# Performance work log

Hardware: AMD Instinct MI355X
Metric: run time of the kernel (lower is better)

## Reference

```python
import jax, jax.numpy as jnp
import numpy as np

ALPHA = 0.0
# tetra edge vertex pairs, same order as the original: (0,1),(0,2),(0,3),(1,2),(1,3),(2,3)
EDGE_PAIRS = np.array([[0, 1], [0, 2], [0, 3], [1, 2], [1, 3], [2, 3]], dtype=np.int32)


def setup_inputs() -> dict:
    key = jax.random.key(0)
    B, N, T = 2, 120000, 600000
    k1, k2 = jax.random.split(key)
    pred = jax.random.normal(k1, (B, N, 4), dtype=jnp.float32)
    tetra = jax.random.randint(k2, (B, T, 4), 0, N, dtype=jnp.int32)
    return {"pred": pred, "tetra": tetra}


def _laplace_tetra(verts, faces):
    # verts: [N,4], faces: [T,4] int. For vertex slot j, contribution is
    # sum_{k != j} (v_k - v_j) = (v0+v1+v2+v3) - 4*v_j ; weight 3 per incidence.
    N = verts.shape[0]
    v = verts[faces]                                  # [T,4,4]
    vsum = jnp.sum(v, axis=1, keepdims=True)          # [T,1,4]
    contrib = (vsum - 4.0 * v).reshape(-1, 4)         # [T*4,4]
    idx = faces.reshape(-1)
    term = jax.ops.segment_sum(contrib, idx, num_segments=N)
    norm = jax.ops.segment_sum(jnp.full(idx.shape, 3.0, verts.dtype), idx, num_segments=N)
    term = term / jnp.clip(norm, 1.0)[:, None]
    return jnp.mean(term ** 2)


def reference(pred, tetra):
    tetra = tetra.astype(jnp.int32)
    # center pred over the point dimension (axis=1)
    pred = pred - jnp.mean(pred, axis=1, keepdims=True)

    def per_batch(pre, tetr):
        L1 = _laplace_tetra(pre, tetr)
        Tetrah = pre[tetr]                             # [T,4,4]
        pa = Tetrah[:, EDGE_PAIRS[:, 0], :]            # [T,6,4] edge endpoint 0
        pb = Tetrah[:, EDGE_PAIRS[:, 1], :]            # [T,6,4] edge endpoint 1
        wa = pa[..., 3]
        wb = pb[..., 3]
        edge = (wa - ALPHA) * (wb - ALPHA)             # [T,6]
        L2 = jnp.mean(wa * wb)
        L3 = jnp.mean((jnp.linalg.norm(pa - pb, axis=-1) - 0.4) ** 2)
        # zero-crossing interpolation: x = (alpha - w0)*m/q + x0
        d = pa - pb                                    # [T,6,4]
        q = d[..., 3]
        safe_q = jnp.where(jnp.abs(q) > 1e-12, q, 1.0)
        t = (ALPHA - wa) / safe_q                      # [T,6]
        pts = pa[..., :3] + t[..., None] * d[..., :3]  # [T,6,3]
        mask = edge < 0                                # valid crossing edges
        pts = jnp.where(mask[..., None], pts, 0.0)
        return L1, L2, L3, pts, mask

    L1, L2, L3, pts, mask = jax.vmap(per_batch)(pred, tetra)
    # losses = [L1, L2, L3, L4] (L4 is always 0 in the original)
    losses = jnp.stack([jnp.mean(L1), jnp.mean(L2), jnp.mean(L3), jnp.zeros((), pred.dtype)])
    return losses, pts, mask
```

## Files before the change

### kernel.cpp

```cpp
#include <hip/hip_runtime.h>


#define VPB 2048
#define VPB_SHIFT 11
#define KMAX 120
#define CAP 49152u
#define NPART 8192
#define FP_BIAS 16.0f
#define FP_SCALE 8.0f
#define FP_INV   0.125f
#define FMASK 0x3FFFULL

typedef float vf4  __attribute__((ext_vector_type(4)));
typedef float vf4u __attribute__((ext_vector_type(4), aligned(4)));
typedef int   vi4  __attribute__((ext_vector_type(4)));

__device__ inline double waveReduce(double v) {
    #pragma unroll
    for (int off = 32; off > 0; off >>= 1) v += __shfl_down(v, off);
    return v;
}

__device__ inline void block_copy_nt(float* __restrict__ dst,
                                     const float* __restrict__ src, int n) {
    int n4 = n >> 2;
    const vf4* s4 = (const vf4*)src;
    vf4u* d4 = (vf4u*)dst;
    for (int i = threadIdx.x; i < n4; i += 256) {
        vf4u v = s4[i];
        __builtin_nontemporal_store(v, d4 + i);
    }
    for (int i = (n4 << 2) + threadIdx.x; i < n; i += 256)
        dst[i] = src[i];
}

__device__ inline void block_copy_u8_nt(float* __restrict__ dst,
                                        const unsigned char* __restrict__ src,
                                        int n) {
    int n4 = n >> 2;
    const uchar4* s4 = (const uchar4*)src;
    vf4u* d4 = (vf4u*)dst;
    for (int i = threadIdx.x; i < n4; i += 256) {
        uchar4 c = s4[i];
        vf4u v = { (float)c.x, (float)c.y, (float)c.z, (float)c.w };
        __builtin_nontemporal_store(v, d4 + i);
    }
    for (int i = (n4 << 2) + threadIdx.x; i < n; i += 256)
        dst[i] = (float)src[i];
}

__global__ __launch_bounds__(256) void mean_kernel(
    const float* __restrict__ pred, double* __restrict__ mpart,
    unsigned* __restrict__ cursors, int N)
{
    if (blockIdx.x == 0 && blockIdx.y == 0 && threadIdx.x < KMAX)
        cursors[threadIdx.x] = 0u;

    const int b = blockIdx.y;
    const float4* p = (const float4*)pred + (size_t)b * N;
    double s0 = 0, s1 = 0, s2 = 0, s3 = 0;
    for (int n = blockIdx.x * blockDim.x + threadIdx.x; n < N;
         n += gridDim.x * blockDim.x) {
        float4 v = p[n];
        s0 += v.x; s1 += v.y; s2 += v.z; s3 += v.w;
    }
    s0 = waveReduce(s0); s1 = waveReduce(s1);
    s2 = waveReduce(s2); s3 = waveReduce(s3);
    __shared__ double mr[4][4];
    int wv = threadIdx.x >> 6;
    if ((threadIdx.x & 63) == 0) {
        mr[wv][0] = s0; mr[wv][1] = s1; mr[wv][2] = s2; mr[wv][3] = s3;
    }
    __syncthreads();
    if (threadIdx.x < 4) {
        double a = mr[0][threadIdx.x] + mr[1][threadIdx.x]
                 + mr[2][threadIdx.x] + mr[3][threadIdx.x];
        mpart[((size_t)b * 32 + blockIdx.x) * 4 + threadIdx.x] = a;
    }
}

__global__ __launch_bounds__(256) void fused_kernel(
    const float* __restrict__ pred, const int* __restrict__ tetra,
    const double* __restrict__ mpart,
    unsigned long long* __restrict__ seg,
    unsigned* __restrict__ cursors,
    unsigned long long* __restrict__ AB,
    double* __restrict__ l2p, double* __restrict__ l3p,
    float* __restrict__ out, int N, int T, int B, int K, int mode)
{
    __shared__ __align__(16) float lds_pts[256 * 18];
    __shared__ __align__(16) unsigned char lds_msk[256 * 6];
    __shared__ double sr[2][4];
    __shared__ unsigned hist[KMAX];
    __shared__ unsigned basei[KMAX];
    __shared__ float bm[4];

    const int b = blockIdx.y;

    if (threadIdx.x < KMAX) hist[threadIdx.x] = 0;
    if (threadIdx.x < 4) {
        double s = 0.0;
        #pragma unroll
        for (int j = 0; j < 32; j++)
            s += mpart[((size_t)b * 32 + j) * 4 + threadIdx.x];
        bm[threadIdx.x] = (float)(s / N);
    }
    __syncthreads();

    const int tbase = blockIdx.x * 256;
    const int t = tbase + threadIdx.x;

    float m0 = bm[0], m1 = bm[1], m2 = bm[2], m3 = bm[3];

    double l2 = 0.0, l3 = 0.0;
    unsigned long long recq = 0, pk = 0;
    int vi[4] = {0, 0, 0, 0};
    unsigned bkt[4] = {0, 0, 0, 0};
    unsigned rnk[4] = {0, 0, 0, 0};
    unsigned rel[4] = {0, 0, 0, 0};
    bool valid = (t < T);

    if (valid) {
        vi4 q4 = __builtin_nontemporal_load((const vi4*)tetra + (size_t)b * T + t);
        vi[0] = q4.x; vi[1] = q4.y; vi[2] = q4.z; vi[3] = q4.w;
        float4 vr[4];
        #pragma unroll
        for (int s = 0; s < 4; s++)
            vr[s] = ((const float4*)pred)[(size_t)b * N + vi[s]];
        float sx = vr[0].x + vr[1].x + vr[2].x + vr[3].x;
        float sy = vr[0].y + vr[1].y + vr[2].y + vr[3].y;
        float sz = vr[0].z + vr[1].z + vr[2].z + vr[3].z;
        float sw = vr[0].w + vr[1].w + vr[2].w + vr[3].w;
        unsigned long long qx = (unsigned long long)((sx + FP_BIAS) * FP_SCALE + 0.5f);
        unsigned long long qy = (unsigned long long)((sy + FP_BIAS) * FP_SCALE + 0.5f);
        unsigned long long qz = (unsigned long long)((sz + FP_BIAS) * FP_SCALE + 0.5f);
        unsigned long long qw = (unsigned long long)((sw + FP_BIAS) * FP_SCALE + 0.5f);
        if (mode == 1) {
            recq = qx | (qy << 9) | (qz << 18) | (qw << 27);
            #pragma unroll
            for (int s = 0; s < 4; s++) {
                unsigned gid = (unsigned)(b * N + vi[s]);
                bkt[s] = gid >> VPB_SHIFT;
                rel[s] = gid & (VPB - 1);
                rnk[s] = atomicAdd(&hist[bkt[s]], 1u);
            }
        } else {
            pk = qx | (qy << 14) | (qz << 28) | (qw << 42) | (1ULL << 56);
        }

        float4 v[4];
        #pragma unroll
        for (int s = 0; s < 4; s++)
            v[s] = make_float4(vr[s].x - m0, vr[s].y - m1, vr[s].z - m2, vr[s].w - m3);
        const int EA[6] = {0, 0, 0, 1, 1, 2};
        const int EB[6] = {1, 2, 3, 2, 3, 3};
        #pragma unroll
        for (int e = 0; e < 6; e++) {
            float4 pa = v[EA[e]], pb = v[EB[e]];
            float wa = pa.w, wb = pb.w;
            float edge = wa * wb;
            float dx = pa.x - pb.x, dy = pa.y - pb.y;
            float dz = pa.z - pb.z, dw = pa.w - pb.w;
            l2 += (double)edge;
            float nr = sqrtf(dx * dx + dy * dy + dz * dz + dw * dw) - 0.4f;
            l3 += (double)(nr * nr);
            float sq = (fabsf(dw) > 1e-12f) ? dw : 1.0f;
            float tt = (0.0f - wa) / sq;
            bool msk = edge < 0.0f;
            lds_pts[threadIdx.x * 18 + e * 3 + 0] = msk ? (pa.x + tt * dx) : 0.0f;
            lds_pts[threadIdx.x * 18 + e * 3 + 1] = msk ? (pa.y + tt * dy) : 0.0f;
            lds_pts[threadIdx.x * 18 + e * 3 + 2] = msk ? (pa.z + tt * dz) : 0.0f;
            lds_msk[threadIdx.x * 6 + e] = msk ? 1 : 0;
        }
    }

    l2 = waveReduce(l2); l3 = waveReduce(l3);
    int wv = threadIdx.x >> 6;
    if ((threadIdx.x & 63) == 0) { sr[0][wv] = l2; sr[1][wv] = l3; }
    __syncthreads();

    if (mode == 1) {
        if (threadIdx.x < K) {
            unsigned h = hist[threadIdx.x];
            basei[threadIdx.x] = h ? atomicAdd(&cursors[threadIdx.x], h) : 0u;
        }
        __syncthreads();
        if (valid) {
            #pragma unroll
            for (int s = 0; s < 4; s++) {
                unsigned slot = basei[bkt[s]] + rnk[s];
                if (slot < CAP)
                    seg[(size_t)bkt[s] * CAP + slot] =
                        recq | ((unsigned long long)rel[s] << 36);
            }
        }
    }

    const int nv = min(256, T - tbase);
    size_t pbase = 4 + ((size_t)b * T + tbase) * 18;
    block_copy_nt(out + pbase, lds_pts, nv * 18);
    size_t mbase = 4 + (size_t)B * T * 18 + ((size_t)b * T + tbase) * 6;
    block_copy_u8_nt(out + mbase, lds_msk, nv * 6);

    if (threadIdx.x == 0) {
        double a = 0, c = 0;
        #pragma unroll
        for (int w = 0; w < 4; w++) { a += sr[0][w]; c += sr[1][w]; }
        int blk = blockIdx.y * gridDim.x + blockIdx.x;
        l2p[blk] = a;
        l3p[blk] = c;
    }

    if (mode == 0 && valid) {
        #pragma unroll
        for (int s = 0; s < 4; s++)
            atomicAdd(&AB[(size_t)b * N + vi[s]], pk);
    }
}

__global__ __launch_bounds__(256) void lap1_kernel(
    const unsigned long long* __restrict__ seg,
    const unsigned* __restrict__ cursors,
    unsigned long long* __restrict__ partial, int M)
{
    __shared__ unsigned long long acc[VPB];
    const int bkt = blockIdx.x;
    const int m = blockIdx.y;

    for (int i = threadIdx.x; i < VPB; i += 256) acc[i] = 0ULL;
    __syncthreads();

    unsigned cnt = min(cursors[bkt], CAP);
    unsigned per = (cnt + M - 1) / M;
    unsigned lo = m * per;
    unsigned hi = min(cnt, lo + per);
    const unsigned long long* s0 = seg + (size_t)bkt * CAP;
    for (unsigned i = lo + threadIdx.x; i < hi; i += 256) {
        unsigned long long r = __builtin_nontemporal_load(&s0[i]);
        unsigned vrel = (unsigned)(r >> 36) & (VPB - 1);
        unsigned long long add =
              (r & 511ULL)
            | (((r >> 9)  & 511ULL) << 14)
            | (((r >> 18) & 511ULL) << 28)
            | (((r >> 27) & 511ULL) << 42)
            | (1ULL << 56);
        atomicAdd(&acc[vrel], add);
    }
    __syncthreads();

    unsigned long long* p = partial + ((size_t)bkt * M + m) * VPB;
    for (int i = threadIdx.x; i < VPB; i += 256) p[i] = acc[i];
}

__global__ __launch_bounds__(256) void lap2_kernel(
    const unsigned long long* __restrict__ partial,
    const float* __restrict__ pred, double* __restrict__ l1p, int BN, int M)
{
    int gid = blockIdx.x * 256 + threadIdx.x;
    double s = 0.0;
    if (gid < BN) {
        int bkt = gid >> VPB_SHIFT;
        int rel = gid & (VPB - 1);
        const unsigned long long* p =
            partial + (size_t)bkt * M * VPB + rel;
        unsigned long long P = 0;
        #pragma unroll 4
        for (int m = 0; m < M; m++) P += p[(size_t)m * VPB];
        int c = (int)(P >> 56);
        float cb = (float)c * FP_BIAS;
        float Sx = (float)(unsigned)( P        & FMASK) * FP_INV - cb;
        float Sy = (float)(unsigned)((P >> 14) & FMASK) * FP_INV - cb;
        float Sz = (float)(unsigned)((P >> 28) & FMASK) * FP_INV - cb;
        float Sw = (float)(unsigned)((P >> 42) & FMASK) * FP_INV - cb;
        float4 v = ((const float4*)pred)[gid];
        float fc = 4.0f * (float)c;
        float tx = Sx - fc * v.x, ty = Sy - fc * v.y;
        float tz = Sz - fc * v.z, tw = Sw - fc * v.w;
        float dn = fmaxf(3.0f * (float)c, 1.0f);
        tx /= dn; ty /= dn; tz /= dn; tw /= dn;
        s = (double)(tx * tx) + (double)(ty * ty)
          + (double)(tz * tz) + (double)(tw * tw);
    }
    s = waveReduce(s);
    __shared__ double sr[4];
    int wv = threadIdx.x >> 6;
    if ((threadIdx.x & 63) == 0) sr[wv] = s;
    __syncthreads();
    if (threadIdx.x == 0) {
        double a = 0;
        #pragma unroll
        for (int w = 0; w < 4; w++) a += sr[w];
        l1p[blockIdx.x] = a;
    }
}

__global__ __launch_bounds__(256) void l1_kernel(
    const unsigned long long* __restrict__ AB, const float* __restrict__ pred,
    double* __restrict__ l1p, int BN)
{
    int i = blockIdx.x * 256 + threadIdx.x;
    double s = 0.0;
    if (i < BN) {
        unsigned long long P = AB[i];
        int c = (int)(P >> 56);
        float cb = (float)c * FP_BIAS;
        float Sx = (float)(unsigned)( P        & FMASK) * FP_INV - cb;
        float Sy = (float)(unsigned)((P >> 14) & FMASK) * FP_INV - cb;
        float Sz = (float)(unsigned)((P >> 28) & FMASK) * FP_INV - cb;
        float Sw = (float)(unsigned)((P >> 42) & FMASK) * FP_INV - cb;
        float4 v = ((const float4*)pred)[i];
        float fc = 4.0f * (float)c;
        float tx = Sx - fc * v.x, ty = Sy - fc * v.y;
        float tz = Sz - fc * v.z, tw = Sw - fc * v.w;
        float dn = fmaxf(3.0f * (float)c, 1.0f);
        tx /= dn; ty /= dn; tz /= dn; tw /= dn;
        s = (double)(tx * tx) + (double)(ty * ty)
          + (double)(tz * tz) + (double)(tw * tw);
    }
    s = waveReduce(s);
    __shared__ double sr[4];
    int wv = threadIdx.x >> 6;
    if ((threadIdx.x & 63) == 0) sr[wv] = s;
    __syncthreads();
    if (threadIdx.x == 0) {
        double a = 0;
        #pragma unroll
        for (int w = 0; w < 4; w++) a += sr[w];
        l1p[blockIdx.x] = a;
    }
}

__global__ __launch_bounds__(256) void finalize_kernel(
    const double* __restrict__ l1p, const double* __restrict__ l2p,
    const double* __restrict__ l3p, float* __restrict__ out,
    double nd1, double nd23, int n1, int n23)
{
    double s1 = 0, s2 = 0, s3 = 0;
    for (int i = threadIdx.x; i < n23; i += 256) { s2 += l2p[i]; s3 += l3p[i]; }
    for (int i = threadIdx.x; i < n1; i += 256) s1 += l1p[i];
    s1 = waveReduce(s1); s2 = waveReduce(s2); s3 = waveReduce(s3);
    __shared__ double sr[3][4];
    int wv = threadIdx.x >> 6;
    if ((threadIdx.x & 63) == 0) { sr[0][wv] = s1; sr[1][wv] = s2; sr[2][wv] = s3; }
    __syncthreads();
    if (threadIdx.x == 0) {
        double a = 0, b = 0, c = 0;
        #pragma unroll
        for (int w = 0; w < 4; w++) { a += sr[0][w]; b += sr[1][w]; c += sr[2][w]; }
        out[0] = (float)(a / nd1);
        out[1] = (float)(b / nd23);
        out[2] = (float)(c / nd23);
        out[3] = 0.0f;
    }
}

extern "C" void kernel_launch(void* const* d_in, const int* in_sizes, int n_in,
                              void* d_out, int out_size, void* d_ws, size_t ws_size,
                              hipStream_t stream) {
    const float* pred = (const float*)d_in[0];
    const int* tetra = (const int*)d_in[1];
    float* out = (float*)d_out;

    const int B = 2;
    const int N = in_sizes[0] / (B * 4);
    const int T = in_sizes[1] / (B * 4);
    const int BN = B * N;
    const int K = (BN + VPB - 1) >> VPB_SHIFT;

    char* ws = (char*)d_ws;
    double* mpart = (double*)ws;
    unsigned* cursors = (unsigned*)(ws + 2048);
    double* l1p = (double*)(ws + 2560);
    double* l2p = (double*)(ws + 68096);
    double* l3p = (double*)(ws + 133632);
    char* dyn = ws + 199168;

    size_t seg_bytes = (size_t)K * CAP * 8;
    int M = 0;
    if ((K <= KMAX) &&
        ws_size >= 199168 + seg_bytes + (size_t)K * 16 * VPB * 8) M = 16;
    else if ((K <= KMAX) &&
        ws_size >= 199168 + seg_bytes + (size_t)K * 8 * VPB * 8) M = 8;

    dim3 mg(32, B);
    dim3 tg((T + 255) / 256, B);
    const int n23 = B * ((T + 255) / 256);
    const int nvb = (BN + 255) / 256;
    double nd1 = (double)BN * 4.0;
    double nd23 = (double)B * (double)T * 6.0;

    if (M > 0) {
        unsigned long long* seg = (unsigned long long*)dyn;
        unsigned long long* partial = (unsigned long long*)(dyn + seg_bytes);
        mean_kernel<<<mg, 256, 0, stream>>>(pred, mpart, cursors, N);
        fused_kernel<<<tg, 256, 0, stream>>>(pred, tetra, mpart, seg, cursors,
                                             nullptr, l2p, l3p, out,
                                             N, T, B, K, 1);
        dim3 lg(K, M);
        lap1_kernel<<<lg, 256, 0, stream>>>(seg, cursors, partial, M);
        lap2_kernel<<<nvb, 256, 0, stream>>>(partial, pred, l1p, BN, M);
        finalize_kernel<<<1, 256, 0, stream>>>(l1p, l2p, l3p, out,
                                               nd1, nd23, nvb, n23);
    } else {
        unsigned long long* AB = (unsigned long long*)dyn;
        (void)hipMemsetAsync(dyn, 0, (size_t)BN * 8, stream);
        mean_kernel<<<mg, 256, 0, stream>>>(pred, mpart, cursors, N);
        fused_kernel<<<tg, 256, 0, stream>>>(pred, tetra, mpart, nullptr, cursors,
                                             AB, l2p, l3p, out,
                                             N, T, B, K, 0);
        l1_kernel<<<nvb, 256, 0, stream>>>(AB, pred, l1p, BN);
        finalize_kernel<<<1, 256, 0, stream>>>(l1p, l2p, l3p, out,
                                               nd1, nd23, nvb, n23);
    }
}
```

Before: 245.4 us.

## Process two tetra tiles per block and overlap gathers with output writes

Each block of fused_kernel now handles 512 tetrahedra instead of 256. Both tiles' gathers are issued up front, and the first tile's output copy-out runs before the second tile's edge computation, reusing the same LDS staging buffers. The scatter of segment records is moved to the end of the kernel, and the cross-block cursor atomics are issued earlier, so gather latency and global write traffic can overlap. It also fixes the Laplacian split factor M at 8 instead of preferring 16, which gives fewer lap1 blocks per bucket. The costs are more register pressure from holding two tiles and a halved grid size, which may reduce occupancy and parallelism.

```diff
diff --git a/kernel.cpp b/kernel.cpp
--- a/kernel.cpp
+++ b/kernel.cpp
@@ -4,8 +4,8 @@
 #define VPB 2048
 #define VPB_SHIFT 11
 #define KMAX 120
+#define LAP_M 8
 #define CAP 49152u
-#define NPART 8192
 #define FP_BIAS 16.0f
 #define FP_SCALE 8.0f
 #define FP_INV   0.125f
@@ -79,6 +79,61 @@
     }
 }
 
+__device__ inline void edge_phase(const float4* vr,
+                                  float m0, float m1, float m2, float m3,
+                                  double& l2, double& l3,
+                                  float* lds_pts, unsigned char* lds_msk)
+{
+    float4 v[4];
+    #pragma unroll
+    for (int s = 0; s < 4; s++)
+        v[s] = make_float4(vr[s].x - m0, vr[s].y - m1, vr[s].z - m2, vr[s].w - m3);
+    const int EA[6] = {0, 0, 0, 1, 1, 2};
+    const int EB[6] = {1, 2, 3, 2, 3, 3};
+    #pragma unroll
+    for (int e = 0; e < 6; e++) {
+        float4 pa = v[EA[e]], pb = v[EB[e]];
+        float wa = pa.w, wb = pb.w;
+        float edge = wa * wb;
+        float dx = pa.x - pb.x, dy = pa.y - pb.y;
+        float dz = pa.z - pb.z, dw = pa.w - pb.w;
+        l2 += (double)edge;
+        float nr = sqrtf(dx * dx + dy * dy + dz * dz + dw * dw) - 0.4f;
+        l3 += (double)(nr * nr);
+        float sq = (fabsf(dw) > 1e-12f) ? dw : 1.0f;
+        float tt = (0.0f - wa) / sq;
+        bool msk = edge < 0.0f;
+        lds_pts[threadIdx.x * 18 + e * 3 + 0] = msk ? (pa.x + tt * dx) : 0.0f;
+        lds_pts[threadIdx.x * 18 + e * 3 + 1] = msk ? (pa.y + tt * dy) : 0.0f;
+        lds_pts[threadIdx.x * 18 + e * 3 + 2] = msk ? (pa.z + tt * dz) : 0.0f;
+        lds_msk[threadIdx.x * 6 + e] = msk ? 1 : 0;
+    }
+}
+
+__device__ inline unsigned long long pack_rec(const float4* vr) {
+    float sx = vr[0].x + vr[1].x + vr[2].x + vr[3].x;
+    float sy = vr[0].y + vr[1].y + vr[2].y + vr[3].y;
+    float sz = vr[0].z + vr[1].z + vr[2].z + vr[3].z;
+    float sw = vr[0].w + vr[1].w + vr[2].w + vr[3].w;
+    unsigned long long qx = (unsigned long long)((sx + FP_BIAS) * FP_SCALE + 0.5f);
+    unsigned long long qy = (unsigned long long)((sy + FP_BIAS) * FP_SCALE + 0.5f);
+    unsigned long long qz = (unsigned long long)((sz + FP_BIAS) * FP_SCALE + 0.5f);
+    unsigned long long qw = (unsigned long long)((sw + FP_BIAS) * FP_SCALE + 0.5f);
+    return qx | (qy << 9) | (qz << 18) | (qw << 27);
+}
+
+__device__ inline unsigned long long pack_ab(const float4* vr) {
+    float sx = vr[0].x + vr[1].x + vr[2].x + vr[3].x;
+    float sy = vr[0].y + vr[1].y + vr[2].y + vr[3].y;
+    float sz = vr[0].z + vr[1].z + vr[2].z + vr[3].z;
+    float sw = vr[0].w + vr[1].w + vr[2].w + vr[3].w;
+    unsigned long long qx = (unsigned long long)((sx + FP_BIAS) * FP_SCALE + 0.5f);
+    unsigned long long qy = (unsigned long long)((sy + FP_BIAS) * FP_SCALE + 0.5f);
+    unsigned long long qz = (unsigned long long)((sz + FP_BIAS) * FP_SCALE + 0.5f);
+    unsigned long long qw = (unsigned long long)((sw + FP_BIAS) * FP_SCALE + 0.5f);
+    return qx | (qy << 14) | (qz << 28) | (qw << 42) | (1ULL << 56);
+}
+
 __global__ __launch_bounds__(256) void fused_kernel(
     const float* __restrict__ pred, const int* __restrict__ tetra,
     const double* __restrict__ mpart,
@@ -107,100 +162,86 @@
     }
     __syncthreads();
 
-    const int tbase = blockIdx.x * 256;
-    const int t = tbase + threadIdx.x;
-
+    const int tbase = blockIdx.x * 512;
+    const int t0 = tbase + threadIdx.x;
+    const int t1 = tbase + 256 + threadIdx.x;
+    const bool v0 = (t0 < T), v1 = (t1 < T);
     float m0 = bm[0], m1 = bm[1], m2 = bm[2], m3 = bm[3];
 
     double l2 = 0.0, l3 = 0.0;
-    unsigned long long recq = 0, pk = 0;
-    int vi[4] = {0, 0, 0, 0};
-    unsigned bkt[4] = {0, 0, 0, 0};
-    unsigned rnk[4] = {0, 0, 0, 0};
-    unsigned rel[4] = {0, 0, 0, 0};
-    bool valid = (t < T);
-
-    if (valid) {
-        vi4 q4 = __builtin_nontemporal_load((const vi4*)tetra + (size_t)b * T + t);
-        vi[0] = q4.x; vi[1] = q4.y; vi[2] = q4.z; vi[3] = q4.w;
-        float4 vr[4];
+    int via[4] = {0,0,0,0}, vib[4] = {0,0,0,0};
+    unsigned rnka[4] = {0,0,0,0}, rnkb[4] = {0,0,0,0};
+    float4 vra[4], vrb[4];
+    unsigned long long recq0 = 0, recq1 = 0;
+
+    if (v0) {
+        vi4 q = __builtin_nontemporal_load((const vi4*)tetra + (size_t)b * T + t0);
+        via[0] = q.x; via[1] = q.y; via[2] = q.z; via[3] = q.w;
         #pragma unroll
         for (int s = 0; s < 4; s++)
-            vr[s] = ((const float4*)pred)[(size_t)b * N + vi[s]];
-        float sx = vr[0].x + vr[1].x + vr[2].x + vr[3].x;
-        float sy = vr[0].y + vr[1].y + vr[2].y + vr[3].y;
-        float sz = vr[0].z + vr[1].z + vr[2].z + vr[3].z;
-        float sw = vr[0].w + vr[1].w + vr[2].w + vr[3].w;
-        unsigned long long qx = (unsigned long long)((sx + FP_BIAS) * FP_SCALE + 0.5f);
-        unsigned long long qy = (unsigned long long)((sy + FP_BIAS) * FP_SCALE + 0.5f);
-        unsigned long long qz = (unsigned long long)((sz + FP_BIAS) * FP_SCALE + 0.5f);
-        unsigned long long qw = (unsigned long long)((sw + FP_BIAS) * FP_SCALE + 0.5f);
-        if (mode == 1) {
-            recq = qx | (qy << 9) | (qz << 18) | (qw << 27);
+            vra[s] = ((const float4*)pred)[(size_t)b * N + via[s]];
+    }
+    if (v1) {
+        vi4 q = __builtin_nontemporal_load((const vi4*)tetra + (size_t)b * T + t1);
+        vib[0] = q.x; vib[1] = q.y; vib[2] = q.z; vib[3] = q.w;
+        #pragma unroll
+        for (int s = 0; s < 4; s++)
+            vrb[s] = ((const float4*)pred)[(size_t)b * N + vib[s]];
+    }
+
+    if (mode == 1) {
+        if (v0) {
             #pragma unroll
             for (int s = 0; s < 4; s++) {
-                unsigned gid = (unsigned)(b * N + vi[s]);
-                bkt[s] = gid >> VPB_SHIFT;
-                rel[s] = gid & (VPB - 1);
-                rnk[s] = atomicAdd(&hist[bkt[s]], 1u);
+                unsigned gid = (unsigned)(b * N + via[s]);
+                rnka[s] = atomicAdd(&hist[gid >> VPB_SHIFT], 1u);
             }
-        } else {
-            pk = qx | (qy << 14) | (qz << 28) | (qw << 42) | (1ULL << 56);
-        }
-
-        float4 v[4];
-        #pragma unroll
-        for (int s = 0; s < 4; s++)
-            v[s] = make_float4(vr[s].x - m0, vr[s].y - m1, vr[s].z - m2, vr[s].w - m3);
-        const int EA[6] = {0, 0, 0, 1, 1, 2};
-        const int EB[6] = {1, 2, 3, 2, 3, 3};
-        #pragma unroll
-        for (int e = 0; e < 6; e++) {
-            float4 pa = v[EA[e]], pb = v[EB[e]];
-            float wa = pa.w, wb = pb.w;
-            float edge = wa * wb;
-            float dx = pa.x - pb.x, dy = pa.y - pb.y;
-            float dz = pa.z - pb.z, dw = pa.w - pb.w;
-            l2 += (double)edge;
-            float nr = sqrtf(dx * dx + dy * dy + dz * dz + dw * dw) - 0.4f;
-            l3 += (double)(nr * nr);
-            float sq = (fabsf(dw) > 1e-12f) ? dw : 1.0f;
-            float tt = (0.0f - wa) / sq;
-            bool msk = edge < 0.0f;
-            lds_pts[threadIdx.x * 18 + e * 3 + 0] = msk ? (pa.x + tt * dx) : 0.0f;
-            lds_pts[threadIdx.x * 18 + e * 3 + 1] = msk ? (pa.y + tt * dy) : 0.0f;
-            lds_pts[threadIdx.x * 18 + e * 3 + 2] = msk ? (pa.z + tt * dz) : 0.0f;
-            lds_msk[threadIdx.x * 6 + e] = msk ? 1 : 0;
-        }
-    }
-
+        }
+        if (v1) {
+            #pragma unroll
+            for (int s = 0; s < 4; s++) {
+                unsigned gid = (unsigned)(b * N + vib[s]);
+                rnkb[s] = atomicAdd(&hist[gid >> VPB_SHIFT], 1u);
+            }
+        }
+    }
+
+    if (v0) {
+        recq0 = (mode == 1) ? pack_rec(vra) : pack_ab(vra);
+        edge_phase(vra, m0, m1, m2, m3, l2, l3, lds_pts, lds_msk);
+    }
+    __syncthreads();
+
+    if (mode == 1 && threadIdx.x < K) {
+        unsigned h = hist[threadIdx.x];
+        basei[threadIdx.x] = h ? atomicAdd(&cursors[threadIdx.x], h) : 0u;
+    }
+
+    const int nv0 = min(256, T - tbase);
+    {
+        size_t pbase = 4 + ((size_t)b * T + tbase) * 18;
+        block_copy_nt(out + pbase, lds_pts, nv0 * 18);
+        size_t mbase = 4 + (size_t)B * T * 18 + ((size_t)b * T + tbase) * 6;
+        block_copy_u8_nt(out + mbase, lds_msk, nv0 * 6);
+    }
+    __syncthreads();
+
+    if (v1) {
+        recq1 = (mode == 1) ? pack_rec(vrb) : pack_ab(vrb);
+        edge_phase(vrb, m0, m1, m2, m3, l2, l3, lds_pts, lds_msk);
+    }
     l2 = waveReduce(l2); l3 = waveReduce(l3);
     int wv = threadIdx.x >> 6;
     if ((threadIdx.x & 63) == 0) { sr[0][wv] = l2; sr[1][wv] = l3; }
     __syncthreads();
 
-    if (mode == 1) {
-        if (threadIdx.x < K) {
-            unsigned h = hist[threadIdx.x];
-            basei[threadIdx.x] = h ? atomicAdd(&cursors[threadIdx.x], h) : 0u;
-        }
-        __syncthreads();
-        if (valid) {
-            #pragma unroll
-            for (int s = 0; s < 4; s++) {
-                unsigned slot = basei[bkt[s]] + rnk[s];
-                if (slot < CAP)
-                    seg[(size_t)bkt[s] * CAP + slot] =
-                        recq | ((unsigned long long)rel[s] << 36);
-            }
-        }
-    }
-
-    const int nv = min(256, T - tbase);
-    size_t pbase = 4 + ((size_t)b * T + tbase) * 18;
-    block_copy_nt(out + pbase, lds_pts, nv * 18);
-    size_t mbase = 4 + (size_t)B * T * 18 + ((size_t)b * T + tbase) * 6;
-    block_copy_u8_nt(out + mbase, lds_msk, nv * 6);
+    const int nv1 = min(256, T - tbase - 256);
+    if (nv1 > 0) {
+        size_t pbase = 4 + ((size_t)b * T + tbase + 256) * 18;
+        block_copy_nt(out + pbase, lds_pts, nv1 * 18);
+        size_t mbase = 4 + (size_t)B * T * 18 + ((size_t)b * T + tbase + 256) * 6;
+        block_copy_u8_nt(out + mbase, lds_msk, nv1 * 6);
+    }
 
     if (threadIdx.x == 0) {
         double a = 0, c = 0;
@@ -211,10 +252,40 @@
         l3p[blk] = c;
     }
 
-    if (mode == 0 && valid) {
-        #pragma unroll
-        for (int s = 0; s < 4; s++)
-            atomicAdd(&AB[(size_t)b * N + vi[s]], pk);
+    if (mode == 1) {
+        if (v0) {
+            #pragma unroll
+            for (int s = 0; s < 4; s++) {
+                unsigned gid = (unsigned)(b * N + via[s]);
+                unsigned bk = gid >> VPB_SHIFT;
+                unsigned slot = basei[bk] + rnka[s];
+                if (slot < CAP)
+                    seg[(size_t)bk * CAP + slot] =
+                        recq0 | ((unsigned long long)(gid & (VPB - 1)) << 36);
+            }
+        }
+        if (v1) {
+            #pragma unroll
+            for (int s = 0; s < 4; s++) {
+                unsigned gid = (unsigned)(b * N + vib[s]);
+                unsigned bk = gid >> VPB_SHIFT;
+                unsigned slot = basei[bk] + rnkb[s];
+                if (slot < CAP)
+                    seg[(size_t)bk * CAP + slot] =
+                        recq1 | ((unsigned long long)(gid & (VPB - 1)) << 36);
+            }
+        }
+    } else {
+        if (v0) {
+            #pragma unroll
+            for (int s = 0; s < 4; s++)
+                atomicAdd(&AB[(size_t)b * N + via[s]], recq0);
+        }
+        if (v1) {
+            #pragma unroll
+            for (int s = 0; s < 4; s++)
+                atomicAdd(&AB[(size_t)b * N + vib[s]], recq1);
+        }
     }
 }
 
@@ -378,13 +449,11 @@
     size_t seg_bytes = (size_t)K * CAP * 8;
     int M = 0;
     if ((K <= KMAX) &&
-        ws_size >= 199168 + seg_bytes + (size_t)K * 16 * VPB * 8) M = 16;
-    else if ((K <= KMAX) &&
-        ws_size >= 199168 + seg_bytes + (size_t)K * 8 * VPB * 8) M = 8;
+        ws_size >= 199168 + seg_bytes + (size_t)K * LAP_M * VPB * 8) M = LAP_M;
 
     dim3 mg(32, B);
-    dim3 tg((T + 255) / 256, B);
-    const int n23 = B * ((T + 255) / 256);
+    dim3 tg((T + 511) / 512, B);
+    const int n23 = B * ((T + 511) / 512);
     const int nvb = (BN + 255) / 256;
     double nd1 = (double)BN * 4.0;
     double nd23 = (double)B * (double)T * 6.0;
```

Result: faster. 221.4 us (-9.8%).
